# Optimization experiments

Measured on AMD Instinct MI355X. Metric: run time of the kernel, lower is better.

Reference implementation:

```python
import jax, jax.numpy as jnp
import numpy as np

B, L, D_INNER, D_STATE, DT_RANK = 1, 1024, 5120, 16, 160


def setup_inputs() -> dict:
    key = jax.random.key(0)
    k0, k1, k2, k3, k4, k5 = jax.random.split(key, 6)
    x = jax.random.normal(k0, (B, L, D_INNER), dtype=jnp.float32)
    # A_log in [0,1) -> A = -exp(A_log) in [-e,-1]: stable decaying recurrence
    A_log = jax.random.uniform(k1, (D_INNER, D_STATE), dtype=jnp.float32)
    D = jax.random.normal(k2, (D_INNER,), dtype=jnp.float32)
    x_proj_w = jax.random.normal(k3, (DT_RANK + 2 * D_STATE, D_INNER), dtype=jnp.float32) * 0.02
    dt_proj_w = jax.random.normal(k4, (D_INNER, DT_RANK), dtype=jnp.float32) * 0.02
    dt_proj_b = jax.random.normal(k5, (D_INNER,), dtype=jnp.float32) * 0.02
    return {"x": x, "A_log": A_log, "D": D, "x_proj_w": x_proj_w,
            "dt_proj_w": dt_proj_w, "dt_proj_b": dt_proj_b}


def reference(x, A_log, D, x_proj_w, dt_proj_w, dt_proj_b):
    # Mamba ssm(): x (b, l, d_inner) -> y (b, l, d_inner)
    A = -jnp.exp(A_log)                                   # (d, n)
    x_dbl = jnp.einsum('bld,ed->ble', x, x_proj_w)        # (b, l, dt_rank+2n)
    dt = x_dbl[..., :DT_RANK]                             # (b, l, r)
    Bm = x_dbl[..., DT_RANK:DT_RANK + D_STATE]            # (b, l, n)
    Cm = x_dbl[..., DT_RANK + D_STATE:]                   # (b, l, n)
    delta = jax.nn.softplus(jnp.einsum('blr,dr->bld', dt, dt_proj_w) + dt_proj_b)

    # discretization (zero-order hold)
    deltaA = jnp.exp(jnp.einsum('bld,dn->bldn', delta, A))        # (b, l, d, n)
    deltaB_u = jnp.einsum('bld,bln,bld->bldn', delta, Bm, x)      # (b, l, d, n)

    def step(h, inp):
        dA_t, dBu_t, c_t = inp          # (b,d,n), (b,d,n), (b,n)
        h = dA_t * h + dBu_t
        y_t = jnp.einsum('bdn,bn->bd', h, c_t)
        return h, y_t

    h0 = jnp.zeros((x.shape[0], D_INNER, D_STATE), dtype=x.dtype)
    xs = (jnp.swapaxes(deltaA, 0, 1),   # (l, b, d, n)
          jnp.swapaxes(deltaB_u, 0, 1),
          jnp.swapaxes(Cm, 0, 1))
    _, ys = jax.lax.scan(step, h0, xs)  # ys: (l, b, d)
    y = jnp.swapaxes(ys, 0, 1)          # (b, l, d)
    return y + x * D
```

## Files before the change

### kernel.cpp

```cpp
#include <hip/hip_runtime.h>
#include <hip/hip_bf16.h>

#define L_SEQ 1024
#define DI    5120
#define DS    16
#define DR    160
#define NE    192
#define NC    16
#define CL    64
#define SPLITK 16
#define KSPLIT (DI / SPLITK)
#define BK    64

#define OFF_P     0
#define SZ_P      (SPLITK * L_SEQ * NE * 4)
#define OFF_XDBL  (OFF_P + SZ_P)
#define SZ_XDBL   (L_SEQ * NE * 4)
#define OFF_DELTA (OFF_XDBL + SZ_XDBL)
#define SZ_DELTA  (L_SEQ * DI * 4)
#define OFF_HEND  (OFF_DELTA + SZ_DELTA)
#define SZ_H      (NC * DS * DI * 4)
#define OFF_APROD (OFF_HEND + SZ_H)
#define WS_END0   (OFF_APROD + SZ_H)
#define OFF_WH    OFF_HEND
#define OFF_WL    (OFF_WH + 1638400)
#define OFF_XH    (OFF_WL + 1638400)
#define OFF_XL    (OFF_XH + 393216)
#define OFF_XPH   WS_END0
#define OFF_XPL   (OFF_XPH + 10485760)
#define OFF_XWH   (OFF_XPL + 10485760)
#define OFF_XWL   (OFF_XWH + 1966080)

typedef short s16x8 __attribute__((ext_vector_type(8)));
typedef float f32x4 __attribute__((ext_vector_type(4)));

__device__ __forceinline__ unsigned short bf_rn(float f) {
  unsigned u = __float_as_uint(f);
  u += 0x7FFFu + ((u >> 16) & 1u);
  return (unsigned short)(u >> 16);
}
__device__ __forceinline__ void split_hilo(float f, unsigned short& h, unsigned short& l) {
  h = bf_rn(f);
  float hf = __uint_as_float(((unsigned)h) << 16);
  l = bf_rn(f - hf);
}

__global__ __launch_bounds__(256) void k_cvt(const float* __restrict__ src,
                                             unsigned short* __restrict__ hi,
                                             unsigned short* __restrict__ lo,
                                             int n4) {
  int i = blockIdx.x * 256 + threadIdx.x;
  if (i >= n4) return;
  int i4 = i * 4;
  float4 v = *(const float4*)&src[i4];
  float f[4] = {v.x, v.y, v.z, v.w};
  ushort4 h, l;
  unsigned short hh, ll;
  split_hilo(f[0], hh, ll); h.x = hh; l.x = ll;
  split_hilo(f[1], hh, ll); h.y = hh; l.y = ll;
  split_hilo(f[2], hh, ll); h.z = hh; l.z = ll;
  split_hilo(f[3], hh, ll); h.w = hh; l.w = ll;
  *(ushort4*)&hi[i4] = h;
  *(ushort4*)&lo[i4] = l;
}

#define AST2 72
__global__ __launch_bounds__(256) void k_xdbl_mfma2(const unsigned short* __restrict__ xph,
                                                    const unsigned short* __restrict__ xpl,
                                                    const unsigned short* __restrict__ wxh,
                                                    const unsigned short* __restrict__ wxl,
                                                    float* __restrict__ part) {
  __shared__ unsigned short sAh[64 * AST2];
  __shared__ unsigned short sAl[64 * AST2];
  const int tid  = threadIdx.x;
  const int lane = tid & 63;
  const int w    = tid >> 6;
  const int wl_  = w >> 1;
  const int we   = w & 1;
  const int l0   = blockIdx.y * 64;
  const int e0   = blockIdx.x * 64 + we * 32;
  const int kb   = blockIdx.z * KSPLIT;
  const int rc   = lane & 15;
  const int kg   = (lane >> 4) * 8;

  f32x4 acc[2][2] = {};
  for (int k0 = 0; k0 < KSPLIT; k0 += BK) {
    __syncthreads();
    for (int idx = tid; idx < 64 * 8; idx += 256) {
      int r = idx >> 3, c8 = (idx & 7) * 8;
      *(s16x8*)&sAh[r * AST2 + c8] = *(const s16x8*)&xph[(size_t)(l0 + r) * DI + kb + k0 + c8];
      *(s16x8*)&sAl[r * AST2 + c8] = *(const s16x8*)&xpl[(size_t)(l0 + r) * DI + kb + k0 + c8];
    }
    __syncthreads();
#pragma unroll
    for (int ks = 0; ks < BK; ks += 32) {
      s16x8 ah[2], al[2], bh[2], bl[2];
#pragma unroll
      for (int mf = 0; mf < 2; ++mf) {
        int row = wl_ * 32 + mf * 16 + rc;
        ah[mf] = *(const s16x8*)&sAh[row * AST2 + ks + kg];
        al[mf] = *(const s16x8*)&sAl[row * AST2 + ks + kg];
      }
#pragma unroll
      for (int nf = 0; nf < 2; ++nf) {
        size_t e = e0 + nf * 16 + rc;
        bh[nf] = *(const s16x8*)&wxh[e * DI + kb + k0 + ks + kg];
        bl[nf] = *(const s16x8*)&wxl[e * DI + kb + k0 + ks + kg];
      }
#pragma unroll
      for (int mf = 0; mf < 2; ++mf)
#pragma unroll
        for (int nf = 0; nf < 2; ++nf) {
          acc[mf][nf] = __builtin_amdgcn_mfma_f32_16x16x32_bf16(ah[mf], bh[nf], acc[mf][nf], 0, 0, 0);
          acc[mf][nf] = __builtin_amdgcn_mfma_f32_16x16x32_bf16(ah[mf], bl[nf], acc[mf][nf], 0, 0, 0);
          acc[mf][nf] = __builtin_amdgcn_mfma_f32_16x16x32_bf16(al[mf], bh[nf], acc[mf][nf], 0, 0, 0);
        }
    }
  }
#pragma unroll
  for (int mf = 0; mf < 2; ++mf)
#pragma unroll
    for (int nf = 0; nf < 2; ++nf)
#pragma unroll
      for (int r = 0; r < 4; ++r) {
        int l = l0 + wl_ * 32 + mf * 16 + (lane >> 4) * 4 + r;
        int e = e0 + nf * 16 + rc;
        part[((size_t)blockIdx.z * L_SEQ + l) * NE + e] = acc[mf][nf][r];
      }
}

__global__ __launch_bounds__(256) void k_xdbl_reduce(const float* __restrict__ part,
                                                     float* __restrict__ xdbl,
                                                     unsigned short* __restrict__ xh,
                                                     unsigned short* __restrict__ xl) {
  int i4 = (blockIdx.x * 256 + threadIdx.x) * 4;
  float4 s = {0.f, 0.f, 0.f, 0.f};
#pragma unroll
  for (int z = 0; z < SPLITK; ++z) {
    float4 p = *(const float4*)&part[(size_t)z * L_SEQ * NE + i4];
    s.x += p.x; s.y += p.y; s.z += p.z; s.w += p.w;
  }
  *(float4*)&xdbl[i4] = s;
  float f[4] = {s.x, s.y, s.z, s.w};
  ushort4 h, l;
  unsigned short hh, ll;
  split_hilo(f[0], hh, ll); h.x = hh; l.x = ll;
  split_hilo(f[1], hh, ll); h.y = hh; l.y = ll;
  split_hilo(f[2], hh, ll); h.z = hh; l.z = ll;
  split_hilo(f[3], hh, ll); h.w = hh; l.w = ll;
  *(ushort4*)&xh[i4] = h;
  *(ushort4*)&xl[i4] = l;
}

#define AST 168
__global__ __launch_bounds__(512) void k_delta_mfma2(const unsigned short* __restrict__ xh,
                                                     const unsigned short* __restrict__ xl,
                                                     const unsigned short* __restrict__ wh,
                                                     const unsigned short* __restrict__ wlo,
                                                     const float* __restrict__ dtb,
                                                     float* __restrict__ delta) {
  __shared__ unsigned short sAh[64 * AST];
  __shared__ unsigned short sAl[64 * AST];
  const int tid  = threadIdx.x;
  const int lane = tid & 63;
  const int w    = tid >> 6;
  const int wl_  = w >> 2;
  const int wd   = w & 3;
  const int l0   = blockIdx.y * 64;
  const int d0   = blockIdx.x * 128 + wd * 32;
  const int rc   = lane & 15;
  const int kg   = (lane >> 4) * 8;

  for (int idx = tid; idx < 64 * 20; idx += 512) {
    int r = idx / 20, c8 = (idx % 20) * 8;
    *(s16x8*)&sAh[r * AST + c8] = *(const s16x8*)&xh[(size_t)(l0 + r) * NE + c8];
    *(s16x8*)&sAl[r * AST + c8] = *(const s16x8*)&xl[(size_t)(l0 + r) * NE + c8];
  }
  __syncthreads();

  f32x4 acc[2][2] = {};
#pragma unroll
  for (int k0 = 0; k0 < DR; k0 += 32) {
    s16x8 ah[2], al[2], bh[2], bl[2];
#pragma unroll
    for (int mf = 0; mf < 2; ++mf) {
      int row = wl_ * 32 + mf * 16 + rc;
      ah[mf] = *(const s16x8*)&sAh[row * AST + k0 + kg];
      al[mf] = *(const s16x8*)&sAl[row * AST + k0 + kg];
    }
#pragma unroll
    for (int nf = 0; nf < 2; ++nf) {
      size_t d = d0 + nf * 16 + rc;
      bh[nf] = *(const s16x8*)&wh[d * DR + k0 + kg];
      bl[nf] = *(const s16x8*)&wlo[d * DR + k0 + kg];
    }
#pragma unroll
    for (int mf = 0; mf < 2; ++mf)
#pragma unroll
      for (int nf = 0; nf < 2; ++nf) {
        acc[mf][nf] = __builtin_amdgcn_mfma_f32_16x16x32_bf16(ah[mf], bh[nf], acc[mf][nf], 0, 0, 0);
        acc[mf][nf] = __builtin_amdgcn_mfma_f32_16x16x32_bf16(ah[mf], bl[nf], acc[mf][nf], 0, 0, 0);
        acc[mf][nf] = __builtin_amdgcn_mfma_f32_16x16x32_bf16(al[mf], bh[nf], acc[mf][nf], 0, 0, 0);
      }
  }
#pragma unroll
  for (int nf = 0; nf < 2; ++nf) {
    int d = d0 + nf * 16 + rc;
    float bias = dtb[d];
#pragma unroll
    for (int mf = 0; mf < 2; ++mf)
#pragma unroll
      for (int r = 0; r < 4; ++r) {
        int l = l0 + wl_ * 32 + mf * 16 + (lane >> 4) * 4 + r;
        float z = acc[mf][nf][r] + bias;
        float sp = fmaxf(z, 0.f) + __logf(1.f + __expf(-fabsf(z)));
        delta[(size_t)l * DI + d] = sp;
      }
  }
}

__global__ __launch_bounds__(256) void k_scan1(const float* __restrict__ x,
                                               const float* __restrict__ delta,
                                               const float* __restrict__ xdbl,
                                               const float* __restrict__ A_log,
                                               float* __restrict__ hend,
                                               float* __restrict__ aprod) {
  const int lane = threadIdx.x & 63;
  const int w    = threadIdx.x >> 6;
  const int d    = blockIdx.x * 64 + w * 16 + (lane & 15);
  const int ng   = lane >> 4;
  const int c    = blockIdx.y;
  __shared__ __align__(16) float sB[CL][DS];
  for (int i = threadIdx.x; i < CL * DS; i += 256) {
    int t = i >> 4, n = i & 15;
    sB[t][n] = xdbl[(size_t)(c * CL + t) * NE + DR + n];
  }
  __syncthreads();
  float4 av = *(const float4*)&A_log[(size_t)d * DS + ng * 4];
  float a[4] = {-__expf(av.x), -__expf(av.y), -__expf(av.z), -__expf(av.w)};
  float h[4] = {0.f, 0.f, 0.f, 0.f};
  float sdl = 0.f;

  const float* dp = &delta[(size_t)(c * CL) * DI + d];
  const float* xp = &x[(size_t)(c * CL) * DI + d];
  float dlb[8], xvb[8];
#pragma unroll
  for (int j = 0; j < 8; ++j) { dlb[j] = dp[(size_t)j * DI]; xvb[j] = xp[(size_t)j * DI]; }
  for (int tt = 0; tt < CL; tt += 8) {
#pragma unroll
    for (int j = 0; j < 8; ++j) {
      float dl = dlb[j], xv = xvb[j];
      int tn = tt + 8 + j;
      if (tn < CL) { dlb[j] = dp[(size_t)tn * DI]; xvb[j] = xp[(size_t)tn * DI]; }
      float du = dl * xv;
      sdl += dl;
      float4 b4 = *(const float4*)&sB[tt + j][ng * 4];
      float bb[4] = {b4.x, b4.y, b4.z, b4.w};
#pragma unroll
      for (int q = 0; q < 4; ++q) {
        float dA = __expf(dl * a[q]);
        h[q] = dA * h[q] + du * bb[q];
      }
    }
  }
#pragma unroll
  for (int q = 0; q < 4; ++q) {
    int n = ng * 4 + q;
    hend[(size_t)(c * DS + n) * DI + d] = h[q];
    aprod[(size_t)(c * DS + n) * DI + d] = __expf(a[q] * sdl);
  }
}

__global__ __launch_bounds__(256) void k_scan2(float* __restrict__ hend,
                                               const float* __restrict__ aprod) {
  int i = blockIdx.x * 256 + threadIdx.x;
  float ap[NC], hv[NC];
#pragma unroll
  for (int c = 0; c < NC; ++c) {
    size_t idx = (size_t)c * DS * DI + i;
    ap[c] = aprod[idx];
    hv[c] = hend[idx];
  }
  float carry = 0.f;
#pragma unroll
  for (int c = 0; c < NC; ++c) {
    size_t idx = (size_t)c * DS * DI + i;
    hend[idx] = carry;
    carry = ap[c] * carry + hv[c];
  }
}

__global__ __launch_bounds__(256) void k_scan3(const float* __restrict__ x,
                                               const float* __restrict__ delta,
                                               const float* __restrict__ xdbl,
                                               const float* __restrict__ A_log,
                                               const float* __restrict__ Dvec,
                                               const float* __restrict__ hstart,
                                               float* __restrict__ out) {
  const int lane = threadIdx.x & 63;
  const int w    = threadIdx.x >> 6;
  const int d    = blockIdx.x * 64 + w * 16 + (lane & 15);
  const int ng   = lane >> 4;
  const int c    = blockIdx.y;
  __shared__ __align__(16) float sB[CL][DS];
  __shared__ __align__(16) float sC[CL][DS];
  for (int i = threadIdx.x; i < CL * DS; i += 256) {
    int t = i >> 4, n = i & 15;
    sB[t][n] = xdbl[(size_t)(c * CL + t) * NE + DR + n];
    sC[t][n] = xdbl[(size_t)(c * CL + t) * NE + DR + DS + n];
  }
  __syncthreads();
  float4 av = *(const float4*)&A_log[(size_t)d * DS + ng * 4];
  float a[4] = {-__expf(av.x), -__expf(av.y), -__expf(av.z), -__expf(av.w)};
  float h[4];
#pragma unroll
  for (int q = 0; q < 4; ++q)
    h[q] = hstart[(size_t)(c * DS + ng * 4 + q) * DI + d];
  const float Dv = Dvec[d];

  const float* dp = &delta[(size_t)(c * CL) * DI + d];
  const float* xp = &x[(size_t)(c * CL) * DI + d];
  float* op = &out[(size_t)(c * CL) * DI + d];
  float dlb[8], xvb[8];
#pragma unroll
  for (int j = 0; j < 8; ++j) { dlb[j] = dp[(size_t)j * DI]; xvb[j] = xp[(size_t)j * DI]; }
  for (int tt = 0; tt < CL; tt += 8) {
#pragma unroll
    for (int j = 0; j < 8; ++j) {
      float dl = dlb[j], xv = xvb[j];
      int tn = tt + 8 + j;
      if (tn < CL) { dlb[j] = dp[(size_t)tn * DI]; xvb[j] = xp[(size_t)tn * DI]; }
      float du = dl * xv;
      float4 b4 = *(const float4*)&sB[tt + j][ng * 4];
      float4 c4 = *(const float4*)&sC[tt + j][ng * 4];
      float bb[4] = {b4.x, b4.y, b4.z, b4.w};
      float cc[4] = {c4.x, c4.y, c4.z, c4.w};
      float y = 0.f;
#pragma unroll
      for (int q = 0; q < 4; ++q) {
        float dA = __expf(dl * a[q]);
        h[q] = dA * h[q] + du * bb[q];
        y += h[q] * cc[q];
      }
      y += __shfl_xor(y, 16, 64);
      y += __shfl_xor(y, 32, 64);
      if (ng == 0) op[(size_t)(tt + j) * DI] = fmaf(xv, Dv, y);
    }
  }
}

extern "C" void kernel_launch(void* const* d_in, const int* in_sizes, int n_in,
                              void* d_out, int out_size, void* d_ws, size_t ws_size,
                              hipStream_t stream) {
  const float* x     = (const float*)d_in[0];
  const float* A_log = (const float*)d_in[1];
  const float* Dvec  = (const float*)d_in[2];
  const float* xw    = (const float*)d_in[3];
  const float* dtw   = (const float*)d_in[4];
  const float* dtb   = (const float*)d_in[5];
  float* out = (float*)d_out;

  char* ws = (char*)d_ws;
  float* part  = (float*)(ws + OFF_P);
  float* xdbl  = (float*)(ws + OFF_XDBL);
  float* delta = (float*)(ws + OFF_DELTA);
  float* hend  = (float*)(ws + OFF_HEND);
  float* aprod = (float*)(ws + OFF_APROD);
  unsigned short* wh  = (unsigned short*)(ws + OFF_WH);
  unsigned short* wl  = (unsigned short*)(ws + OFF_WL);
  unsigned short* xh  = (unsigned short*)(ws + OFF_XH);
  unsigned short* xl  = (unsigned short*)(ws + OFF_XL);
  unsigned short* xph = (unsigned short*)(ws + OFF_XPH);
  unsigned short* xpl = (unsigned short*)(ws + OFF_XPL);
  unsigned short* wxh = (unsigned short*)(ws + OFF_XWH);
  unsigned short* wxl = (unsigned short*)(ws + OFF_XWL);

  k_cvt<<<5120, 256, 0, stream>>>(x, xph, xpl, L_SEQ * DI / 4);
  k_cvt<<<960, 256, 0, stream>>>(xw, wxh, wxl, NE * DI / 4);
  k_cvt<<<800, 256, 0, stream>>>(dtw, wh, wl, DI * DR / 4);
  k_xdbl_mfma2<<<dim3(3, 16, SPLITK), 256, 0, stream>>>(xph, xpl, wxh, wxl, part);
  k_xdbl_reduce<<<192, 256, 0, stream>>>(part, xdbl, xh, xl);
  k_delta_mfma2<<<dim3(40, 16), 512, 0, stream>>>(xh, xl, wh, wl, dtb, delta);
  k_scan1<<<dim3(80, NC), 256, 0, stream>>>(x, delta, xdbl, A_log, hend, aprod);
  k_scan2<<<320, 256, 0, stream>>>(hend, aprod);
  k_scan3<<<dim3(80, NC), 256, 0, stream>>>(x, delta, xdbl, A_log, Dvec, hend, out);
}
```

Baseline: 107.2 us.

## Give each scan thread all 16 states and halve the chunk length

The chunked-scan kernels now map one thread to one channel holding all 16 state values, instead of spreading a channel's states over four lane groups. This removes the redundant delta/x loads across those groups and the cross-lane shuffle reduction for y. Chunks shrink from 64 to 32 steps, which doubles the chunk count to restore some of the parallelism lost by the new mapping. The inner exp uses exp2f with A pre-scaled by log2(e). In exchange, each thread needs more registers, there are half as many threads in total, and the carry-propagation pass and its buffers now handle twice as many chunks.

Result: slower. 147.7 us (+37.8%).

```diff
diff --git a/kernel.cpp b/kernel.cpp
--- a/kernel.cpp
+++ b/kernel.cpp
@@ -6,11 +6,12 @@
 #define DS    16
 #define DR    160
 #define NE    192
-#define NC    16
-#define CL    64
+#define NC    32
+#define CL    32
 #define SPLITK 16
 #define KSPLIT (DI / SPLITK)
 #define BK    64
+#define LOG2E 1.44269504088896340736f
 
 #define OFF_P     0
 #define SZ_P      (SPLITK * L_SEQ * NE * 4)
@@ -225,49 +226,56 @@
                                                const float* __restrict__ A_log,
                                                float* __restrict__ hend,
                                                float* __restrict__ aprod) {
-  const int lane = threadIdx.x & 63;
-  const int w    = threadIdx.x >> 6;
-  const int d    = blockIdx.x * 64 + w * 16 + (lane & 15);
-  const int ng   = lane >> 4;
-  const int c    = blockIdx.y;
+  const int d = blockIdx.x * 256 + threadIdx.x;
+  const int c = blockIdx.y;
   __shared__ __align__(16) float sB[CL][DS];
   for (int i = threadIdx.x; i < CL * DS; i += 256) {
     int t = i >> 4, n = i & 15;
     sB[t][n] = xdbl[(size_t)(c * CL + t) * NE + DR + n];
   }
   __syncthreads();
-  float4 av = *(const float4*)&A_log[(size_t)d * DS + ng * 4];
-  float a[4] = {-__expf(av.x), -__expf(av.y), -__expf(av.z), -__expf(av.w)};
-  float h[4] = {0.f, 0.f, 0.f, 0.f};
+  float aL[DS], h[DS];
+#pragma unroll
+  for (int q4 = 0; q4 < DS; q4 += 4) {
+    float4 av = *(const float4*)&A_log[(size_t)d * DS + q4];
+    aL[q4 + 0] = -__expf(av.x) * LOG2E;
+    aL[q4 + 1] = -__expf(av.y) * LOG2E;
+    aL[q4 + 2] = -__expf(av.z) * LOG2E;
+    aL[q4 + 3] = -__expf(av.w) * LOG2E;
+  }
+#pragma unroll
+  for (int q = 0; q < DS; ++q) h[q] = 0.f;
   float sdl = 0.f;
 
   const float* dp = &delta[(size_t)(c * CL) * DI + d];
   const float* xp = &x[(size_t)(c * CL) * DI + d];
-  float dlb[8], xvb[8];
-#pragma unroll
-  for (int j = 0; j < 8; ++j) { dlb[j] = dp[(size_t)j * DI]; xvb[j] = xp[(size_t)j * DI]; }
-  for (int tt = 0; tt < CL; tt += 8) {
-#pragma unroll
-    for (int j = 0; j < 8; ++j) {
+  float dlb[4], xvb[4];
+#pragma unroll
+  for (int j = 0; j < 4; ++j) { dlb[j] = dp[(size_t)j * DI]; xvb[j] = xp[(size_t)j * DI]; }
+  for (int tt = 0; tt < CL; tt += 4) {
+    bool pf = (tt + 4 < CL);
+#pragma unroll
+    for (int j = 0; j < 4; ++j) {
       float dl = dlb[j], xv = xvb[j];
-      int tn = tt + 8 + j;
-      if (tn < CL) { dlb[j] = dp[(size_t)tn * DI]; xvb[j] = xp[(size_t)tn * DI]; }
+      if (pf) { int tn = tt + 4 + j; dlb[j] = dp[(size_t)tn * DI]; xvb[j] = xp[(size_t)tn * DI]; }
       float du = dl * xv;
       sdl += dl;
-      float4 b4 = *(const float4*)&sB[tt + j][ng * 4];
-      float bb[4] = {b4.x, b4.y, b4.z, b4.w};
-#pragma unroll
-      for (int q = 0; q < 4; ++q) {
-        float dA = __expf(dl * a[q]);
-        h[q] = dA * h[q] + du * bb[q];
-      }
-    }
-  }
-#pragma unroll
-  for (int q = 0; q < 4; ++q) {
-    int n = ng * 4 + q;
-    hend[(size_t)(c * DS + n) * DI + d] = h[q];
-    aprod[(size_t)(c * DS + n) * DI + d] = __expf(a[q] * sdl);
+#pragma unroll
+      for (int q4 = 0; q4 < DS; q4 += 4) {
+        float4 b4 = *(const float4*)&sB[tt + j][q4];
+        float bb[4] = {b4.x, b4.y, b4.z, b4.w};
+#pragma unroll
+        for (int u = 0; u < 4; ++u) {
+          float dA = exp2f(dl * aL[q4 + u]);
+          h[q4 + u] = dA * h[q4 + u] + du * bb[u];
+        }
+      }
+    }
+  }
+#pragma unroll
+  for (int q = 0; q < DS; ++q) {
+    hend[(size_t)(c * DS + q) * DI + d] = h[q];
+    aprod[(size_t)(c * DS + q) * DI + d] = exp2f(aL[q] * sdl);
   }
 }
 
@@ -297,11 +305,8 @@
                                                const float* __restrict__ Dvec,
                                                const float* __restrict__ hstart,
                                                float* __restrict__ out) {
-  const int lane = threadIdx.x & 63;
-  const int w    = threadIdx.x >> 6;
-  const int d    = blockIdx.x * 64 + w * 16 + (lane & 15);
-  const int ng   = lane >> 4;
-  const int c    = blockIdx.y;
+  const int d = blockIdx.x * 256 + threadIdx.x;
+  const int c = blockIdx.y;
   __shared__ __align__(16) float sB[CL][DS];
   __shared__ __align__(16) float sC[CL][DS];
   for (int i = threadIdx.x; i < CL * DS; i += 256) {
@@ -310,41 +315,49 @@
     sC[t][n] = xdbl[(size_t)(c * CL + t) * NE + DR + DS + n];
   }
   __syncthreads();
-  float4 av = *(const float4*)&A_log[(size_t)d * DS + ng * 4];
-  float a[4] = {-__expf(av.x), -__expf(av.y), -__expf(av.z), -__expf(av.w)};
-  float h[4];
-#pragma unroll
-  for (int q = 0; q < 4; ++q)
-    h[q] = hstart[(size_t)(c * DS + ng * 4 + q) * DI + d];
+  float aL[DS], h[DS];
+#pragma unroll
+  for (int q4 = 0; q4 < DS; q4 += 4) {
+    float4 av = *(const float4*)&A_log[(size_t)d * DS + q4];
+    aL[q4 + 0] = -__expf(av.x) * LOG2E;
+    aL[q4 + 1] = -__expf(av.y) * LOG2E;
+    aL[q4 + 2] = -__expf(av.z) * LOG2E;
+    aL[q4 + 3] = -__expf(av.w) * LOG2E;
+  }
+#pragma unroll
+  for (int q = 0; q < DS; ++q)
+    h[q] = hstart[(size_t)(c * DS + q) * DI + d];
   const float Dv = Dvec[d];
 
   const float* dp = &delta[(size_t)(c * CL) * DI + d];
   const float* xp = &x[(size_t)(c * CL) * DI + d];
   float* op = &out[(size_t)(c * CL) * DI + d];
-  float dlb[8], xvb[8];
-#pragma unroll
-  for (int j = 0; j < 8; ++j) { dlb[j] = dp[(size_t)j * DI]; xvb[j] = xp[(size_t)j * DI]; }
-  for (int tt = 0; tt < CL; tt += 8) {
-#pragma unroll
-    for (int j = 0; j < 8; ++j) {
+  float dlb[4], xvb[4];
+#pragma unroll
+  for (int j = 0; j < 4; ++j) { dlb[j] = dp[(size_t)j * DI]; xvb[j] = xp[(size_t)j * DI]; }
+  for (int tt = 0; tt < CL; tt += 4) {
+    bool pf = (tt + 4 < CL);
+#pragma unroll
+    for (int j = 0; j < 4; ++j) {
       float dl = dlb[j], xv = xvb[j];
-      int tn = tt + 8 + j;
-      if (tn < CL) { dlb[j] = dp[(size_t)tn * DI]; xvb[j] = xp[(size_t)tn * DI]; }
+      if (pf) { int tn = tt + 4 + j; dlb[j] = dp[(size_t)tn * DI]; xvb[j] = xp[(size_t)tn * DI]; }
       float du = dl * xv;
-      float4 b4 = *(const float4*)&sB[tt + j][ng * 4];
-      float4 c4 = *(const float4*)&sC[tt + j][ng * 4];
-      float bb[4] = {b4.x, b4.y, b4.z, b4.w};
-      float cc[4] = {c4.x, c4.y, c4.z, c4.w};
-      float y = 0.f;
-#pragma unroll
-      for (int q = 0; q < 4; ++q) {
-        float dA = __expf(dl * a[q]);
-        h[q] = dA * h[q] + du * bb[q];
-        y += h[q] * cc[q];
-      }
-      y += __shfl_xor(y, 16, 64);
-      y += __shfl_xor(y, 32, 64);
-      if (ng == 0) op[(size_t)(tt + j) * DI] = fmaf(xv, Dv, y);
+      float yp[4] = {0.f, 0.f, 0.f, 0.f};
+#pragma unroll
+      for (int q4 = 0; q4 < DS; q4 += 4) {
+        float4 b4 = *(const float4*)&sB[tt + j][q4];
+        float4 c4 = *(const float4*)&sC[tt + j][q4];
+        float bb[4] = {b4.x, b4.y, b4.z, b4.w};
+        float cc[4] = {c4.x, c4.y, c4.z, c4.w};
+#pragma unroll
+        for (int u = 0; u < 4; ++u) {
+          float dA = exp2f(dl * aL[q4 + u]);
+          h[q4 + u] = dA * h[q4 + u] + du * bb[u];
+          yp[u] += h[q4 + u] * cc[u];
+        }
+      }
+      float y = (yp[0] + yp[1]) + (yp[2] + yp[3]);
+      op[(size_t)(tt + j) * DI] = fmaf(xv, Dv, y);
     }
   }
 }
@@ -381,7 +394,7 @@
   k_xdbl_mfma2<<<dim3(3, 16, SPLITK), 256, 0, stream>>>(xph, xpl, wxh, wxl, part);
   k_xdbl_reduce<<<192, 256, 0, stream>>>(part, xdbl, xh, xl);
   k_delta_mfma2<<<dim3(40, 16), 512, 0, stream>>>(xh, xl, wh, wl, dtb, delta);
-  k_scan1<<<dim3(80, NC), 256, 0, stream>>>(x, delta, xdbl, A_log, hend, aprod);
+  k_scan1<<<dim3(20, NC), 256, 0, stream>>>(x, delta, xdbl, A_log, hend, aprod);
   k_scan2<<<320, 256, 0, stream>>>(hend, aprod);
-  k_scan3<<<dim3(80, NC), 256, 0, stream>>>(x, delta, xdbl, A_log, Dvec, hend, out);
-}
+  k_scan3<<<dim3(20, NC), 256, 0, stream>>>(x, delta, xdbl, A_log, Dvec, hend, out);
+}
```

## Fuse chunked selective scan into one cooperative kernel with grid syncs

Applied to the files above, without the earlier changes.

Replaces the three scan kernels with a single cooperative kernel. It computes per-chunk end states, does the cross-chunk carry pass and the output pass, separated by grid-wide syncs. Chunk length drops to 32 with twice as many chunks, and each thread now owns all 16 states of one channel. The delta-projection kernel now writes delta and x interleaved as float2, so the scans do one load per step, and the exponentials use exp2f with prescaled A. The aim is to cut launch overhead and the second read of delta and x. The cost is fewer threads, heavier per-thread register and LDS use, grid-sync latency and a larger workspace, with the old three-kernel path kept as a fallback.

Result: slower. 131.1 us (+22.3%).

```diff
diff --git a/kernel.cpp b/kernel.cpp
--- a/kernel.cpp
+++ b/kernel.cpp
@@ -1,16 +1,20 @@
 #include <hip/hip_runtime.h>
 #include <hip/hip_bf16.h>
+#include <hip/hip_cooperative_groups.h>
+
+namespace cg = cooperative_groups;
 
 #define L_SEQ 1024
 #define DI    5120
 #define DS    16
 #define DR    160
 #define NE    192
-#define NC    16
-#define CL    64
+#define NC    32
+#define CL    32
 #define SPLITK 16
 #define KSPLIT (DI / SPLITK)
 #define BK    64
+#define LOG2E 1.44269504088896340736f
 
 #define OFF_P     0
 #define SZ_P      (SPLITK * L_SEQ * NE * 4)
@@ -30,6 +34,7 @@
 #define OFF_XPL   (OFF_XPH + 10485760)
 #define OFF_XWH   (OFF_XPL + 10485760)
 #define OFF_XWL   (OFF_XWH + 1966080)
+#define OFF_ZB    (OFF_XWL + 1966080)
 
 typedef short s16x8 __attribute__((ext_vector_type(8)));
 typedef float f32x4 __attribute__((ext_vector_type(4)));
@@ -158,7 +163,8 @@
                                                      const unsigned short* __restrict__ wh,
                                                      const unsigned short* __restrict__ wlo,
                                                      const float* __restrict__ dtb,
-                                                     float* __restrict__ delta) {
+                                                     const float* __restrict__ x,
+                                                     float2* __restrict__ zbuf) {
   __shared__ unsigned short sAh[64 * AST];
   __shared__ unsigned short sAl[64 * AST];
   const int tid  = threadIdx.x;
@@ -214,17 +220,124 @@
         int l = l0 + wl_ * 32 + mf * 16 + (lane >> 4) * 4 + r;
         float z = acc[mf][nf][r] + bias;
         float sp = fmaxf(z, 0.f) + __logf(1.f + __expf(-fabsf(z)));
-        delta[(size_t)l * DI + d] = sp;
-      }
-  }
-}
-
-__global__ __launch_bounds__(256) void k_scan1(const float* __restrict__ x,
-                                               const float* __restrict__ delta,
-                                               const float* __restrict__ xdbl,
-                                               const float* __restrict__ A_log,
-                                               float* __restrict__ hend,
-                                               float* __restrict__ aprod) {
+        float xv = x[(size_t)l * DI + d];
+        zbuf[(size_t)l * DI + d] = make_float2(sp, xv);
+      }
+  }
+}
+
+__global__ __launch_bounds__(512, 4) void k_scan_fused2(const float2* __restrict__ zbuf,
+                                                        const float* __restrict__ xdbl,
+                                                        const float* __restrict__ A_log,
+                                                        const float* __restrict__ Dvec,
+                                                        float* __restrict__ hend,
+                                                        float* __restrict__ aprod,
+                                                        float* __restrict__ out) {
+  const int tid = threadIdx.x;
+  const int d   = blockIdx.x * 512 + tid;
+  const int c   = blockIdx.y;
+  __shared__ __align__(16) float sB[CL][DS];
+  __shared__ __align__(16) float sC[CL][DS];
+  __shared__ float sX[CL][512];
+
+  {
+    int i = tid;
+    int t = i >> 4, n = i & 15;
+    sB[t][n] = xdbl[(size_t)(c * CL + t) * NE + DR + n];
+    sC[t][n] = xdbl[(size_t)(c * CL + t) * NE + DR + DS + n];
+  }
+
+  float aL[DS];
+#pragma unroll
+  for (int q4 = 0; q4 < DS; q4 += 4) {
+    float4 av = *(const float4*)&A_log[(size_t)d * DS + q4];
+    aL[q4 + 0] = -__expf(av.x) * LOG2E;
+    aL[q4 + 1] = -__expf(av.y) * LOG2E;
+    aL[q4 + 2] = -__expf(av.z) * LOG2E;
+    aL[q4 + 3] = -__expf(av.w) * LOG2E;
+  }
+
+  const float2* zp = &zbuf[(size_t)(c * CL) * DI + d];
+  float dl[CL];
+#pragma unroll
+  for (int j = 0; j < CL; ++j) {
+    float2 z = zp[(size_t)j * DI];
+    dl[j] = z.x;
+    sX[j][tid] = z.y;
+  }
+  __syncthreads();
+
+  float h[DS];
+#pragma unroll
+  for (int q = 0; q < DS; ++q) h[q] = 0.f;
+  float sdl = 0.f;
+#pragma unroll
+  for (int j = 0; j < CL; ++j) {
+    float xv = sX[j][tid];
+    float du = dl[j] * xv;
+    sdl += dl[j];
+#pragma unroll
+    for (int q = 0; q < DS; ++q) {
+      float dA = exp2f(dl[j] * aL[q]);
+      h[q] = dA * h[q] + du * sB[j][q];
+    }
+  }
+#pragma unroll
+  for (int q = 0; q < DS; ++q) {
+    hend[(size_t)(c * DS + q) * DI + d] = h[q];
+    aprod[(size_t)(c * DS + q) * DI + d] = exp2f(aL[q] * sdl);
+  }
+
+  __threadfence();
+  cg::this_grid().sync();
+
+  {
+    int fid = (blockIdx.y * gridDim.x + blockIdx.x) * 512 + tid;
+    if (fid < DS * DI) {
+      float carry = 0.f;
+#pragma unroll 1
+      for (int c2 = 0; c2 < NC; ++c2) {
+        size_t idx = (size_t)c2 * DS * DI + fid;
+        float ap = aprod[idx];
+        float hv = hend[idx];
+        hend[idx] = carry;
+        carry = ap * carry + hv;
+      }
+    }
+  }
+  __threadfence();
+  cg::this_grid().sync();
+
+#pragma unroll
+  for (int q = 0; q < DS; ++q)
+    h[q] = hend[(size_t)(c * DS + q) * DI + d];
+  const float Dv = Dvec[d];
+  float* op = &out[(size_t)(c * CL) * DI + d];
+#pragma unroll
+  for (int j = 0; j < CL; ++j) {
+    float dlj = dl[j];
+    float xv = sX[j][tid];
+    float du = dlj * xv;
+    float yp[4] = {0.f, 0.f, 0.f, 0.f};
+#pragma unroll
+    for (int q4 = 0; q4 < DS; q4 += 4) {
+#pragma unroll
+      for (int u = 0; u < 4; ++u) {
+        float dA = exp2f(dlj * aL[q4 + u]);
+        h[q4 + u] = dA * h[q4 + u] + du * sB[j][q4 + u];
+        yp[u] += h[q4 + u] * sC[j][q4 + u];
+      }
+    }
+    float y = (yp[0] + yp[1]) + (yp[2] + yp[3]);
+    op[(size_t)j * DI] = fmaf(xv, Dv, y);
+  }
+}
+
+__global__ __launch_bounds__(256) void k_scan1f(const float2* __restrict__ zbuf,
+                                                const float* __restrict__ xdbl,
+                                                const float* __restrict__ A_log,
+                                                float* __restrict__ hend,
+                                                float* __restrict__ aprod) {
   const int lane = threadIdx.x & 63;
   const int w    = threadIdx.x >> 6;
   const int d    = blockIdx.x * 64 + w * 16 + (lane & 15);
@@ -237,28 +350,27 @@
   }
   __syncthreads();
   float4 av = *(const float4*)&A_log[(size_t)d * DS + ng * 4];
-  float a[4] = {-__expf(av.x), -__expf(av.y), -__expf(av.z), -__expf(av.w)};
+  float aL[4] = {-__expf(av.x) * LOG2E, -__expf(av.y) * LOG2E,
+                 -__expf(av.z) * LOG2E, -__expf(av.w) * LOG2E};
   float h[4] = {0.f, 0.f, 0.f, 0.f};
   float sdl = 0.f;
-
-  const float* dp = &delta[(size_t)(c * CL) * DI + d];
-  const float* xp = &x[(size_t)(c * CL) * DI + d];
-  float dlb[8], xvb[8];
-#pragma unroll
-  for (int j = 0; j < 8; ++j) { dlb[j] = dp[(size_t)j * DI]; xvb[j] = xp[(size_t)j * DI]; }
+  const float2* zp = &zbuf[(size_t)(c * CL) * DI + d];
+  float2 zb[8];
+#pragma unroll
+  for (int j = 0; j < 8; ++j) zb[j] = zp[(size_t)j * DI];
   for (int tt = 0; tt < CL; tt += 8) {
 #pragma unroll
     for (int j = 0; j < 8; ++j) {
-      float dl = dlb[j], xv = xvb[j];
+      float dl = zb[j].x, xv = zb[j].y;
       int tn = tt + 8 + j;
-      if (tn < CL) { dlb[j] = dp[(size_t)tn * DI]; xvb[j] = xp[(size_t)tn * DI]; }
+      if (tn < CL) zb[j] = zp[(size_t)tn * DI];
       float du = dl * xv;
       sdl += dl;
       float4 b4 = *(const float4*)&sB[tt + j][ng * 4];
       float bb[4] = {b4.x, b4.y, b4.z, b4.w};
 #pragma unroll
       for (int q = 0; q < 4; ++q) {
-        float dA = __expf(dl * a[q]);
+        float dA = exp2f(dl * aL[q]);
         h[q] = dA * h[q] + du * bb[q];
       }
     }
@@ -267,36 +379,30 @@
   for (int q = 0; q < 4; ++q) {
     int n = ng * 4 + q;
     hend[(size_t)(c * DS + n) * DI + d] = h[q];
-    aprod[(size_t)(c * DS + n) * DI + d] = __expf(a[q] * sdl);
-  }
-}
-
-__global__ __launch_bounds__(256) void k_scan2(float* __restrict__ hend,
-                                               const float* __restrict__ aprod) {
+    aprod[(size_t)(c * DS + n) * DI + d] = exp2f(aL[q] * sdl);
+  }
+}
+
+__global__ __launch_bounds__(256) void k_scan2f(float* __restrict__ hend,
+                                                const float* __restrict__ aprod) {
   int i = blockIdx.x * 256 + threadIdx.x;
-  float ap[NC], hv[NC];
-#pragma unroll
+  float carry = 0.f;
+#pragma unroll 1
   for (int c = 0; c < NC; ++c) {
     size_t idx = (size_t)c * DS * DI + i;
-    ap[c] = aprod[idx];
-    hv[c] = hend[idx];
-  }
-  float carry = 0.f;
-#pragma unroll
-  for (int c = 0; c < NC; ++c) {
-    size_t idx = (size_t)c * DS * DI + i;
+    float ap = aprod[idx];
+    float hv = hend[idx];
     hend[idx] = carry;
-    carry = ap[c] * carry + hv[c];
-  }
-}
-
-__global__ __launch_bounds__(256) void k_scan3(const float* __restrict__ x,
-                                               const float* __restrict__ delta,
-                                               const float* __restrict__ xdbl,
-                                               const float* __restrict__ A_log,
-                                               const float* __restrict__ Dvec,
-                                               const float* __restrict__ hstart,
-                                               float* __restrict__ out) {
+    carry = ap * carry + hv;
+  }
+}
+
+__global__ __launch_bounds__(256) void k_scan3f(const float2* __restrict__ zbuf,
+                                                const float* __restrict__ xdbl,
+                                                const float* __restrict__ A_log,
+                                                const float* __restrict__ Dvec,
+                                                const float* __restrict__ hstart,
+                                                float* __restrict__ out) {
   const int lane = threadIdx.x & 63;
   const int w    = threadIdx.x >> 6;
   const int d    = blockIdx.x * 64 + w * 16 + (lane & 15);
@@ -311,25 +417,24 @@
   }
   __syncthreads();
   float4 av = *(const float4*)&A_log[(size_t)d * DS + ng * 4];
-  float a[4] = {-__expf(av.x), -__expf(av.y), -__expf(av.z), -__expf(av.w)};
+  float aL[4] = {-__expf(av.x) * LOG2E, -__expf(av.y) * LOG2E,
+                 -__expf(av.z) * LOG2E, -__expf(av.w) * LOG2E};
   float h[4];
 #pragma unroll
   for (int q = 0; q < 4; ++q)
     h[q] = hstart[(size_t)(c * DS + ng * 4 + q) * DI + d];
   const float Dv = Dvec[d];
-
-  const float* dp = &delta[(size_t)(c * CL) * DI + d];
-  const float* xp = &x[(size_t)(c * CL) * DI + d];
+  const float2* zp = &zbuf[(size_t)(c * CL) * DI + d];
   float* op = &out[(size_t)(c * CL) * DI + d];
-  float dlb[8], xvb[8];
-#pragma unroll
-  for (int j = 0; j < 8; ++j) { dlb[j] = dp[(size_t)j * DI]; xvb[j] = xp[(size_t)j * DI]; }
+  float2 zb[8];
+#pragma unroll
+  for (int j = 0; j < 8; ++j) zb[j] = zp[(size_t)j * DI];
   for (int tt = 0; tt < CL; tt += 8) {
 #pragma unroll
     for (int j = 0; j < 8; ++j) {
-      float dl = dlb[j], xv = xvb[j];
+      float dl = zb[j].x, xv = zb[j].y;
       int tn = tt + 8 + j;
-      if (tn < CL) { dlb[j] = dp[(size_t)tn * DI]; xvb[j] = xp[(size_t)tn * DI]; }
+      if (tn < CL) zb[j] = zp[(size_t)tn * DI];
       float du = dl * xv;
       float4 b4 = *(const float4*)&sB[tt + j][ng * 4];
       float4 c4 = *(const float4*)&sC[tt + j][ng * 4];
@@ -338,7 +443,7 @@
       float y = 0.f;
 #pragma unroll
       for (int q = 0; q < 4; ++q) {
-        float dA = __expf(dl * a[q]);
+        float dA = exp2f(dl * aL[q]);
         h[q] = dA * h[q] + du * bb[q];
         y += h[q] * cc[q];
       }
@@ -363,7 +468,6 @@
   char* ws = (char*)d_ws;
   float* part  = (float*)(ws + OFF_P);
   float* xdbl  = (float*)(ws + OFF_XDBL);
-  float* delta = (float*)(ws + OFF_DELTA);
   float* hend  = (float*)(ws + OFF_HEND);
   float* aprod = (float*)(ws + OFF_APROD);
   unsigned short* wh  = (unsigned short*)(ws + OFF_WH);
@@ -374,14 +478,29 @@
   unsigned short* xpl = (unsigned short*)(ws + OFF_XPL);
   unsigned short* wxh = (unsigned short*)(ws + OFF_XWH);
   unsigned short* wxl = (unsigned short*)(ws + OFF_XWL);
+  float2* zbuf = (float2*)(ws + OFF_ZB);
 
   k_cvt<<<5120, 256, 0, stream>>>(x, xph, xpl, L_SEQ * DI / 4);
   k_cvt<<<960, 256, 0, stream>>>(xw, wxh, wxl, NE * DI / 4);
   k_cvt<<<800, 256, 0, stream>>>(dtw, wh, wl, DI * DR / 4);
   k_xdbl_mfma2<<<dim3(3, 16, SPLITK), 256, 0, stream>>>(xph, xpl, wxh, wxl, part);
   k_xdbl_reduce<<<192, 256, 0, stream>>>(part, xdbl, xh, xl);
-  k_delta_mfma2<<<dim3(40, 16), 512, 0, stream>>>(xh, xl, wh, wl, dtb, delta);
-  k_scan1<<<dim3(80, NC), 256, 0, stream>>>(x, delta, xdbl, A_log, hend, aprod);
-  k_scan2<<<320, 256, 0, stream>>>(hend, aprod);
-  k_scan3<<<dim3(80, NC), 256, 0, stream>>>(x, delta, xdbl, A_log, Dvec, hend, out);
-}
+  k_delta_mfma2<<<dim3(40, 16), 512, 0, stream>>>(xh, xl, wh, wl, dtb, x, zbuf);
+
+  int coopAttr = 0, ncu = 0, nb = 0;
+  hipDeviceGetAttribute(&coopAttr, hipDeviceAttributeCooperativeLaunch, 0);
+  hipDeviceGetAttribute(&ncu, hipDeviceAttributeMultiprocessorCount, 0);
+  hipOccupancyMaxActiveBlocksPerMultiprocessor(&nb, (const void*)k_scan_fused2, 512, 0);
+  bool useCoop = (coopAttr != 0) && ((long)nb * ncu >= 320);
+
+  if (useCoop) {
+    void* args[] = {(void*)&zbuf, (void*)&xdbl, (void*)&A_log, (void*)&Dvec,
+                    (void*)&hend, (void*)&aprod, (void*)&out};
+    hipError_t ce = hipLaunchCooperativeKernel((void*)k_scan_fused2, dim3(10, NC),
+                                               dim3(512), args, 0, stream);
+    if (ce == hipSuccess) return;
+  }
+  k_scan1f<<<dim3(80, NC), 256, 0, stream>>>(zbuf, xdbl, A_log, hend, aprod);
+  k_scan2f<<<320, 256, 0, stream>>>(hend, aprod);
+  k_scan3f<<<dim3(80, NC), 256, 0, stream>>>(zbuf, xdbl, A_log, Dvec, hend, out);
+}
```

## Fuse delta GEMM with chunk scan pass and interleave delta with x for scan3

Applied to the files above, without the earlier changes.

Merges the delta projection kernel with the first chunked-scan pass. Delta tiles now stay in shared memory and the per-chunk scan reads them from there instead of from a global delta buffer. The fused kernel also writes an interleaved (delta, x) float2 buffer so scan3 issues one load stream instead of two. Exponentials switch to exp2f with a LOG2E-prescaled A. The trade-off is that the scan phase now runs on only 640 blocks with 512 threads each, and the extra float2 buffer adds global write traffic.

Result: slower. 120.8 us (+12.7%).

```diff
diff --git a/kernel.cpp b/kernel.cpp
--- a/kernel.cpp
+++ b/kernel.cpp
@@ -11,25 +11,21 @@
 #define SPLITK 16
 #define KSPLIT (DI / SPLITK)
 #define BK    64
+#define LOG2E 1.44269504088896340736f
 
 #define OFF_P     0
-#define SZ_P      (SPLITK * L_SEQ * NE * 4)
-#define OFF_XDBL  (OFF_P + SZ_P)
-#define SZ_XDBL   (L_SEQ * NE * 4)
-#define OFF_DELTA (OFF_XDBL + SZ_XDBL)
-#define SZ_DELTA  (L_SEQ * DI * 4)
-#define OFF_HEND  (OFF_DELTA + SZ_DELTA)
-#define SZ_H      (NC * DS * DI * 4)
-#define OFF_APROD (OFF_HEND + SZ_H)
-#define WS_END0   (OFF_APROD + SZ_H)
-#define OFF_WH    OFF_HEND
-#define OFF_WL    (OFF_WH + 1638400)
-#define OFF_XH    (OFF_WL + 1638400)
-#define OFF_XL    (OFF_XH + 393216)
-#define OFF_XPH   WS_END0
-#define OFF_XPL   (OFF_XPH + 10485760)
-#define OFF_XWH   (OFF_XPL + 10485760)
-#define OFF_XWL   (OFF_XWH + 1966080)
+#define OFF_XDBL  12582912
+#define OFF_WH    13369344
+#define OFF_WL    15007744
+#define OFF_XH    16646144
+#define OFF_XL    17039360
+#define OFF_XPH   17432576
+#define OFF_XPL   27918336
+#define OFF_XWH   38404096
+#define OFF_XWL   40370176
+#define OFF_ZB    42336256
+#define OFF_HEND  84279296
+#define OFF_APROD 89522176
 
 typedef short s16x8 __attribute__((ext_vector_type(8)));
 typedef float f32x4 __attribute__((ext_vector_type(4)));
@@ -153,21 +149,30 @@
 }
 
 #define AST 168
-__global__ __launch_bounds__(512) void k_delta_mfma2(const unsigned short* __restrict__ xh,
+#define DST 129
+__global__ __launch_bounds__(512) void k_delta_scan1(const unsigned short* __restrict__ xh,
                                                      const unsigned short* __restrict__ xl,
                                                      const unsigned short* __restrict__ wh,
                                                      const unsigned short* __restrict__ wlo,
                                                      const float* __restrict__ dtb,
-                                                     float* __restrict__ delta) {
-  __shared__ unsigned short sAh[64 * AST];
-  __shared__ unsigned short sAl[64 * AST];
+                                                     const float* __restrict__ x,
+                                                     const float* __restrict__ xdbl,
+                                                     const float* __restrict__ A_log,
+                                                     float2* __restrict__ zbuf,
+                                                     float* __restrict__ hend,
+                                                     float* __restrict__ aprod) {
+  __shared__ __align__(16) unsigned char smem[64 * AST * 2 * 2];
+  unsigned short* sAh = (unsigned short*)smem;
+  unsigned short* sAl = sAh + 64 * AST;
   const int tid  = threadIdx.x;
   const int lane = tid & 63;
   const int w    = tid >> 6;
   const int wl_  = w >> 2;
   const int wd   = w & 3;
-  const int l0   = blockIdx.y * 64;
-  const int d0   = blockIdx.x * 128 + wd * 32;
+  const int c    = blockIdx.y;
+  const int l0   = c * 64;
+  const int d0b  = blockIdx.x * 128;
+  const int d0   = d0b + wd * 32;
   const int rc   = lane & 15;
   const int kg   = (lane >> 4) * 8;
 
@@ -203,62 +208,60 @@
         acc[mf][nf] = __builtin_amdgcn_mfma_f32_16x16x32_bf16(al[mf], bh[nf], acc[mf][nf], 0, 0, 0);
       }
   }
+  __syncthreads();
+
+  float* sDelta = (float*)smem;
+  float* sB     = (float*)(smem + 64 * DST * 4);
+  for (int i = tid; i < 64 * 16; i += 512) {
+    int t = i >> 4, n = i & 15;
+    sB[i] = xdbl[(size_t)(l0 + t) * NE + DR + n];
+  }
 #pragma unroll
   for (int nf = 0; nf < 2; ++nf) {
     int d = d0 + nf * 16 + rc;
+    int dloc = d - d0b;
     float bias = dtb[d];
 #pragma unroll
     for (int mf = 0; mf < 2; ++mf)
 #pragma unroll
       for (int r = 0; r < 4; ++r) {
-        int l = l0 + wl_ * 32 + mf * 16 + (lane >> 4) * 4 + r;
+        int lloc = wl_ * 32 + mf * 16 + (lane >> 4) * 4 + r;
+        int l = l0 + lloc;
         float z = acc[mf][nf][r] + bias;
         float sp = fmaxf(z, 0.f) + __logf(1.f + __expf(-fabsf(z)));
-        delta[(size_t)l * DI + d] = sp;
-      }
-  }
-}
-
-__global__ __launch_bounds__(256) void k_scan1(const float* __restrict__ x,
-                                               const float* __restrict__ delta,
-                                               const float* __restrict__ xdbl,
-                                               const float* __restrict__ A_log,
-                                               float* __restrict__ hend,
-                                               float* __restrict__ aprod) {
-  const int lane = threadIdx.x & 63;
-  const int w    = threadIdx.x >> 6;
-  const int d    = blockIdx.x * 64 + w * 16 + (lane & 15);
-  const int ng   = lane >> 4;
-  const int c    = blockIdx.y;
-  __shared__ __align__(16) float sB[CL][DS];
-  for (int i = threadIdx.x; i < CL * DS; i += 256) {
-    int t = i >> 4, n = i & 15;
-    sB[t][n] = xdbl[(size_t)(c * CL + t) * NE + DR + n];
+        float xv = x[(size_t)l * DI + d];
+        sDelta[lloc * DST + dloc] = sp;
+        zbuf[(size_t)l * DI + d] = make_float2(sp, xv);
+      }
   }
   __syncthreads();
+
+  const int dloc = tid & 127;
+  const int ng   = tid >> 7;
+  const int d    = d0b + dloc;
   float4 av = *(const float4*)&A_log[(size_t)d * DS + ng * 4];
-  float a[4] = {-__expf(av.x), -__expf(av.y), -__expf(av.z), -__expf(av.w)};
+  float aL[4] = {-__expf(av.x) * LOG2E, -__expf(av.y) * LOG2E,
+                 -__expf(av.z) * LOG2E, -__expf(av.w) * LOG2E};
   float h[4] = {0.f, 0.f, 0.f, 0.f};
   float sdl = 0.f;
-
-  const float* dp = &delta[(size_t)(c * CL) * DI + d];
-  const float* xp = &x[(size_t)(c * CL) * DI + d];
-  float dlb[8], xvb[8];
-#pragma unroll
-  for (int j = 0; j < 8; ++j) { dlb[j] = dp[(size_t)j * DI]; xvb[j] = xp[(size_t)j * DI]; }
-  for (int tt = 0; tt < CL; tt += 8) {
-#pragma unroll
-    for (int j = 0; j < 8; ++j) {
-      float dl = dlb[j], xv = xvb[j];
-      int tn = tt + 8 + j;
-      if (tn < CL) { dlb[j] = dp[(size_t)tn * DI]; xvb[j] = xp[(size_t)tn * DI]; }
+  const float* xp = &x[(size_t)l0 * DI + d];
+  float xb[4];
+#pragma unroll
+  for (int j = 0; j < 4; ++j) xb[j] = xp[(size_t)j * DI];
+  for (int tt = 0; tt < CL; tt += 4) {
+    bool pf = (tt + 4 < CL);
+#pragma unroll
+    for (int j = 0; j < 4; ++j) {
+      float xv = xb[j];
+      if (pf) xb[j] = xp[(size_t)(tt + 4 + j) * DI];
+      float dl = sDelta[(tt + j) * DST + dloc];
       float du = dl * xv;
       sdl += dl;
-      float4 b4 = *(const float4*)&sB[tt + j][ng * 4];
+      float4 b4 = *(const float4*)&sB[(tt + j) * 16 + ng * 4];
       float bb[4] = {b4.x, b4.y, b4.z, b4.w};
 #pragma unroll
       for (int q = 0; q < 4; ++q) {
-        float dA = __expf(dl * a[q]);
+        float dA = exp2f(dl * aL[q]);
         h[q] = dA * h[q] + du * bb[q];
       }
     }
@@ -267,7 +270,7 @@
   for (int q = 0; q < 4; ++q) {
     int n = ng * 4 + q;
     hend[(size_t)(c * DS + n) * DI + d] = h[q];
-    aprod[(size_t)(c * DS + n) * DI + d] = __expf(a[q] * sdl);
+    aprod[(size_t)(c * DS + n) * DI + d] = exp2f(aL[q] * sdl);
   }
 }
 
@@ -290,8 +293,7 @@
   }
 }
 
-__global__ __launch_bounds__(256) void k_scan3(const float* __restrict__ x,
-                                               const float* __restrict__ delta,
+__global__ __launch_bounds__(256) void k_scan3(const float2* __restrict__ zbuf,
                                                const float* __restrict__ xdbl,
                                                const float* __restrict__ A_log,
                                                const float* __restrict__ Dvec,
@@ -311,25 +313,24 @@
   }
   __syncthreads();
   float4 av = *(const float4*)&A_log[(size_t)d * DS + ng * 4];
-  float a[4] = {-__expf(av.x), -__expf(av.y), -__expf(av.z), -__expf(av.w)};
+  float aL[4] = {-__expf(av.x) * LOG2E, -__expf(av.y) * LOG2E,
+                 -__expf(av.z) * LOG2E, -__expf(av.w) * LOG2E};
   float h[4];
 #pragma unroll
   for (int q = 0; q < 4; ++q)
     h[q] = hstart[(size_t)(c * DS + ng * 4 + q) * DI + d];
   const float Dv = Dvec[d];
-
-  const float* dp = &delta[(size_t)(c * CL) * DI + d];
-  const float* xp = &x[(size_t)(c * CL) * DI + d];
+  const float2* zp = &zbuf[(size_t)(c * CL) * DI + d];
   float* op = &out[(size_t)(c * CL) * DI + d];
-  float dlb[8], xvb[8];
-#pragma unroll
-  for (int j = 0; j < 8; ++j) { dlb[j] = dp[(size_t)j * DI]; xvb[j] = xp[(size_t)j * DI]; }
+  float2 zb[8];
+#pragma unroll
+  for (int j = 0; j < 8; ++j) zb[j] = zp[(size_t)j * DI];
   for (int tt = 0; tt < CL; tt += 8) {
 #pragma unroll
     for (int j = 0; j < 8; ++j) {
-      float dl = dlb[j], xv = xvb[j];
+      float dl = zb[j].x, xv = zb[j].y;
       int tn = tt + 8 + j;
-      if (tn < CL) { dlb[j] = dp[(size_t)tn * DI]; xvb[j] = xp[(size_t)tn * DI]; }
+      if (tn < CL) zb[j] = zp[(size_t)tn * DI];
       float du = dl * xv;
       float4 b4 = *(const float4*)&sB[tt + j][ng * 4];
       float4 c4 = *(const float4*)&sC[tt + j][ng * 4];
@@ -338,7 +339,7 @@
       float y = 0.f;
 #pragma unroll
       for (int q = 0; q < 4; ++q) {
-        float dA = __expf(dl * a[q]);
+        float dA = exp2f(dl * aL[q]);
         h[q] = dA * h[q] + du * bb[q];
         y += h[q] * cc[q];
       }
@@ -363,7 +364,6 @@
   char* ws = (char*)d_ws;
   float* part  = (float*)(ws + OFF_P);
   float* xdbl  = (float*)(ws + OFF_XDBL);
-  float* delta = (float*)(ws + OFF_DELTA);
   float* hend  = (float*)(ws + OFF_HEND);
   float* aprod = (float*)(ws + OFF_APROD);
   unsigned short* wh  = (unsigned short*)(ws + OFF_WH);
@@ -374,14 +374,15 @@
   unsigned short* xpl = (unsigned short*)(ws + OFF_XPL);
   unsigned short* wxh = (unsigned short*)(ws + OFF_XWH);
   unsigned short* wxl = (unsigned short*)(ws + OFF_XWL);
+  float2* zbuf = (float2*)(ws + OFF_ZB);
 
   k_cvt<<<5120, 256, 0, stream>>>(x, xph, xpl, L_SEQ * DI / 4);
   k_cvt<<<960, 256, 0, stream>>>(xw, wxh, wxl, NE * DI / 4);
   k_cvt<<<800, 256, 0, stream>>>(dtw, wh, wl, DI * DR / 4);
   k_xdbl_mfma2<<<dim3(3, 16, SPLITK), 256, 0, stream>>>(xph, xpl, wxh, wxl, part);
   k_xdbl_reduce<<<192, 256, 0, stream>>>(part, xdbl, xh, xl);
-  k_delta_mfma2<<<dim3(40, 16), 512, 0, stream>>>(xh, xl, wh, wl, dtb, delta);
-  k_scan1<<<dim3(80, NC), 256, 0, stream>>>(x, delta, xdbl, A_log, hend, aprod);
+  k_delta_scan1<<<dim3(40, 16), 512, 0, stream>>>(xh, xl, wh, wl, dtb, x, xdbl,
+                                                  A_log, zbuf, hend, aprod);
   k_scan2<<<320, 256, 0, stream>>>(hend, aprod);
-  k_scan3<<<dim3(80, NC), 256, 0, stream>>>(x, delta, xdbl, A_log, Dvec, hend, out);
-}
+  k_scan3<<<dim3(80, 16), 256, 0, stream>>>(zbuf, xdbl, A_log, Dvec, hend, out);
+}
```
